# Kernel tuning notes

Hardware: AMD Instinct MI355X
Metric: run time of the kernel (lower is better)

Reference implementation:

```python
import jax, jax.numpy as jnp
import numpy as np

NUM_HEADS = 12
HEAD_DIM = 64
HIDDEN = NUM_HEADS * HEAD_DIM


def setup_inputs() -> dict:
    key = jax.random.key(0)
    ks = jax.random.split(key, 10)
    B, S, N_ROT = 8, 1374, 1369
    s = 0.02
    return {
        "hidden_states": jax.random.normal(ks[0], (B, S, HIDDEN), jnp.float32),
        "sin": jax.random.normal(ks[1], (N_ROT, HEAD_DIM), jnp.float32),
        "cos": jax.random.normal(ks[2], (N_ROT, HEAD_DIM), jnp.float32),
        "Wq": jax.random.normal(ks[3], (HIDDEN, HIDDEN), jnp.float32) * s,
        "bq": jax.random.normal(ks[4], (HIDDEN,), jnp.float32) * s,
        "Wk": jax.random.normal(ks[5], (HIDDEN, HIDDEN), jnp.float32) * s,
        "Wv": jax.random.normal(ks[6], (HIDDEN, HIDDEN), jnp.float32) * s,
        "bv": jax.random.normal(ks[7], (HIDDEN,), jnp.float32) * s,
        "Wp": jax.random.normal(ks[8], (HIDDEN, HIDDEN), jnp.float32) * s,
        "bp": jax.random.normal(ks[9], (HIDDEN,), jnp.float32) * s,
    }


def _rotate_half(x):
    x1, x2 = jnp.split(x, 2, axis=-1)
    return jnp.concatenate([-x2, x1], axis=-1)


def _rope_apply(x, sin, cos):
    return x * cos + _rotate_half(x) * sin


def reference(hidden_states, sin, cos, Wq, bq, Wk, Wv, bv, Wp, bp):
    B, S, _ = hidden_states.shape
    scaling = HEAD_DIM ** -0.5

    def to_heads(x):  # [B,S,HIDDEN] -> [B,H,S,D]
        return x.reshape(B, S, NUM_HEADS, HEAD_DIM).transpose(0, 2, 1, 3)

    q = to_heads(hidden_states @ Wq.T + bq)
    k = to_heads(hidden_states @ Wk.T)  # no key bias (mask_k_bias)
    v = to_heads(hidden_states @ Wv.T + bv)

    # RoPE only on patch tokens (prefix = cls + register tokens untouched)
    prefix = S - sin.shape[-2]
    q = jnp.concatenate([q[:, :, :prefix], _rope_apply(q[:, :, prefix:], sin, cos)], axis=2)
    k = jnp.concatenate([k[:, :, :prefix], _rope_apply(k[:, :, prefix:], sin, cos)], axis=2)

    # eager attention: softmax in float32, no mask, no dropout (eval)
    scores = jnp.einsum("bhqd,bhkd->bhqk", q, k) * scaling
    probs = jax.nn.softmax(scores.astype(jnp.float32), axis=-1).astype(q.dtype)
    ctx = jnp.einsum("bhqk,bhkd->bqhd", probs, v).reshape(B, S, HIDDEN)
    return ctx @ Wp.T + bp
```

## Files before the change

### kernel.cpp

```cpp
#include <hip/hip_runtime.h>
#include <stdint.h>

typedef unsigned short u16;
typedef unsigned int u32;
typedef u16 u16x8 __attribute__((ext_vector_type(8)));
typedef __bf16 bf16x8 __attribute__((ext_vector_type(8)));
typedef float f32x4 __attribute__((ext_vector_type(4)));

#define S_LEN 1374
#define S_PAD 1408
#define PRE_TOK 5
#define HID 768
#define NH 12
#define MPAD 11008

__device__ __forceinline__ u16 f2bf(float f) {
    union { float f; u32 u; } v; v.f = f;
    u32 r = v.u + 0x7fffu + ((v.u >> 16) & 1u);
    return (u16)(r >> 16);
}
__device__ __forceinline__ bf16x8 as_bf(u16x8 v) { bf16x8 r; __builtin_memcpy(&r, &v, 16); return r; }
__device__ __forceinline__ bf16x8 lds_load8(const u16* p) {
    u16x8 t = *(const u16x8*)p;
    return as_bf(t);
}
__device__ __forceinline__ u32 cvtpk_bf16(float lo, float hi) {
    u32 r;
    asm("v_cvt_pk_bf16_f32 %0, %1, %2" : "=v"(r) : "v"(lo), "v"(hi));
    return r;
}
__device__ __forceinline__ float fexp2(float x) {
    float r;
    asm("v_exp_f32 %0, %1" : "=v"(r) : "v"(x));
    return r;
}
__device__ __forceinline__ void gload16(void* lds, const void* g) {
    unsigned int __attribute__((address_space(1)))* gp =
        (unsigned int __attribute__((address_space(1)))*)(unsigned long long)g;
    unsigned int __attribute__((address_space(3)))* lp =
        (unsigned int __attribute__((address_space(3)))*)(unsigned int)(unsigned long long)lds;
    __builtin_amdgcn_global_load_lds(gp, lp, 16, 0, 0);
}
__device__ __forceinline__ int xcd_swz(int orig, int nwg) {
    int qd = nwg >> 3, rd = nwg & 7;
    int xcd = orig & 7, rem = orig >> 3;
    return (xcd < rd ? xcd * (qd + 1) : rd * (qd + 1) + (xcd - rd) * qd) + rem;
}


__global__ __launch_bounds__(256) void pack_x(const float* __restrict__ X, u16* __restrict__ Xb) {
    size_t i = (size_t)blockIdx.x * 256 + threadIdx.x;
    size_t e = i * 8;
    const size_t TOT = (size_t)10992 * HID;
    u16x8 o = {0,0,0,0,0,0,0,0};
    if (e < TOT) {
        f32x4 a = *(const f32x4*)(X + e);
        f32x4 b = *(const f32x4*)(X + e + 4);
#pragma unroll
        for (int j = 0; j < 4; ++j) { o[j] = f2bf(a[j]); o[4 + j] = f2bf(b[j]); }
    }
    *(u16x8*)(Xb + e) = o;
}

__global__ __launch_bounds__(256) void pack_w(
    const float* __restrict__ Wq, const float* __restrict__ Wk, const float* __restrict__ Wv,
    const float* __restrict__ Wp, const float* __restrict__ bq, const float* __restrict__ bv,
    u16* __restrict__ wqkv, u16* __restrict__ wpb, float* __restrict__ bqkv)
{
    int g = blockIdx.x * 256 + threadIdx.x;
    const int QKV8 = 2304 * HID / 8;
    const int P8 = HID * HID / 8;
    if (g < QKV8) {
        int e = g * 8;
        int row = e / HID, col = e - row * HID;
        const float* src = (row < 768) ? (Wq + (size_t)row * HID + col)
                         : (row < 1536) ? (Wk + (size_t)(row - 768) * HID + col)
                                        : (Wv + (size_t)(row - 1536) * HID + col);
        u16x8 o;
#pragma unroll
        for (int j = 0; j < 8; ++j) o[j] = f2bf(src[j]);
        *(u16x8*)(wqkv + e) = o;
    } else if (g < QKV8 + P8) {
        int e = (g - QKV8) * 8;
        u16x8 o;
#pragma unroll
        for (int j = 0; j < 8; ++j) o[j] = f2bf(Wp[e + j]);
        *(u16x8*)(wpb + e) = o;
    }
    if (g < 288) {
        int e = g * 8;
#pragma unroll
        for (int j = 0; j < 8; ++j) {
            int c = e + j;
            bqkv[c] = (c < 768) ? bq[c] : (c < 1536 ? 0.f : bv[c - 1536]);
        }
    }
}


template <int EPI>
__global__ __launch_bounds__(512) void gemm_nt(
    const u16* __restrict__ A, const u16* __restrict__ B, const float* __restrict__ bias,
    float* __restrict__ Yf, u16* __restrict__ Qh, u16* __restrict__ Kh,
    u16* __restrict__ Yv, const float* __restrict__ SN, const float* __restrict__ CS,
    int N, int K, int nx, int nwg)
{
    __shared__ u16 As[128 * 64];
    __shared__ u16 Bs[256 * 64];
    int tid = threadIdx.x;
    int w = tid >> 6, l = tid & 63;
    int fr = l & 15, fg = l >> 4;
    int wg = xcd_swz(blockIdx.x, nwg);
    int col0 = (wg % nx) * 256;
    int row0 = (wg / nx) * 128;
    int wr = (w >> 2) * 64;
    int wc = (w & 3) * 64;

    f32x4 zero4 = {0.f, 0.f, 0.f, 0.f};
    f32x4 acc[4][4];
#pragma unroll
    for (int m = 0; m < 4; ++m)
#pragma unroll
        for (int n = 0; n < 4; ++n) acc[m][n] = zero4;

    int arow[2], aoff[2];
#pragma unroll
    for (int i = 0; i < 2; ++i) {
        int sbyte = (i * 512 + tid) * 16;
        int r = sbyte >> 7;
        int ir = (sbyte & 127) ^ ((r & 7) << 4);
        arow[i] = r; aoff[i] = ir >> 1;
    }
    int brow[4], boff[4];
#pragma unroll
    for (int i = 0; i < 4; ++i) {
        int sbyte = (i * 512 + tid) * 16;
        int r = sbyte >> 7;
        int ir = (sbyte & 127) ^ ((r & 7) << 4);
        brow[i] = r; boff[i] = ir >> 1;
    }

    for (int kt = 0; kt < K; kt += 64) {
#pragma unroll
        for (int i = 0; i < 2; ++i)
            gload16((char*)As + i * 8192 + w * 1024,
                    A + (size_t)(row0 + arow[i]) * K + kt + aoff[i]);
#pragma unroll
        for (int i = 0; i < 4; ++i)
            gload16((char*)Bs + i * 8192 + w * 1024,
                    B + (size_t)(col0 + brow[i]) * K + kt + boff[i]);
        __syncthreads();
#pragma unroll
        for (int c = 0; c < 2; ++c) {
            bf16x8 af[4], bfr[4];
#pragma unroll
            for (int m = 0; m < 4; ++m) {
                int r = wr + m * 16 + fr;
                int byte_ = (c * 64 + fg * 16) ^ ((r & 7) << 4);
                af[m] = lds_load8(As + r * 64 + (byte_ >> 1));
            }
#pragma unroll
            for (int n = 0; n < 4; ++n) {
                int r = wc + n * 16 + fr;
                int byte_ = (c * 64 + fg * 16) ^ ((r & 7) << 4);
                bfr[n] = lds_load8(Bs + r * 64 + (byte_ >> 1));
            }
#pragma unroll
            for (int m = 0; m < 4; ++m)
#pragma unroll
                for (int n = 0; n < 4; ++n)
                    acc[m][n] = __builtin_amdgcn_mfma_f32_16x16x32_bf16(af[m], bfr[n], acc[m][n], 0, 0, 0);
        }
        __syncthreads();
    }

    if (EPI == 1) {
#pragma unroll
        for (int m = 0; m < 4; ++m)
#pragma unroll
            for (int n = 0; n < 4; ++n) {
                int gn = col0 + wc + n * 16 + fr;
                float bvv = bias[gn];
#pragma unroll
                for (int j = 0; j < 4; ++j) {
                    int gm = row0 + wr + m * 16 + fg * 4 + j;
                    if (gm < 10992) Yf[(size_t)gm * N + gn] = acc[m][n][j] + bvv;
                }
            }
    } else {
        int sect = col0 >= 1536 ? 2 : (col0 >= 768 ? 1 : 0);
        if (sect == 2) {
#pragma unroll
            for (int m = 0; m < 4; ++m)
#pragma unroll
                for (int n = 0; n < 4; ++n) {
                    int gn = col0 + wc + n * 16 + fr;
                    float bvv = bias[gn];
#pragma unroll
                    for (int j = 0; j < 4; ++j) {
                        int gm = row0 + wr + m * 16 + fg * 4 + j;
                        if (gm < 10992)
                            Yv[(size_t)gm * HID + (gn - 1536)] = f2bf(acc[m][n][j] + bvv);
                    }
                }
        } else {
            u16* H = sect ? Kh : Qh;
            const float QS = sect ? 1.f : 0.125f * 1.44269504088896f;
            int hh = ((col0 + wc) >> 6) - sect * NH;
            float bv4[4];
#pragma unroll
            for (int n = 0; n < 4; ++n) bv4[n] = bias[col0 + wc + n * 16 + fr];
#pragma unroll
            for (int m = 0; m < 4; ++m)
#pragma unroll
                for (int j = 0; j < 4; ++j) {
                    int gm = row0 + wr + m * 16 + fg * 4 + j;
                    if (gm < 10992) {
                        int b = gm / 1374, s = gm - b * 1374;
                        size_t ob = ((size_t)(b * NH + hh) * S_PAD + s) * 64;
#pragma unroll
                        for (int n2 = 0; n2 < 2; ++n2) {
                            int d = n2 * 16 + fr;
                            float v1 = acc[m][n2][j] + bv4[n2];
                            float v2 = acc[m][n2 + 2][j] + bv4[n2 + 2];
                            float a1 = v1, a2 = v2;
                            if (s >= PRE_TOK) {
                                size_t rr = (size_t)(s - PRE_TOK) * 64;
                                float c1 = CS[rr + d], s1 = SN[rr + d];
                                float c2 = CS[rr + d + 32], s2 = SN[rr + d + 32];
                                a1 = v1 * c1 - v2 * s1;
                                a2 = v2 * c2 + v1 * s2;
                            }
                            H[ob + d]      = f2bf(a1 * QS);
                            H[ob + d + 32] = f2bf(a2 * QS);
                        }
                    }
                }
        }
    }
}


__global__ __launch_bounds__(256) void v_pack(const u16* __restrict__ Yv, u16* __restrict__ Vt) {
    int st = blockIdx.x, bh = blockIdx.y;
    int b = bh / NH, h = bh - b * NH;
    int tid = threadIdx.x;
    int sl = tid >> 2, dg = (tid & 3) * 8;
    int s = st * 64 + sl;
    __shared__ u16 vtile[64 * 64];

    u16x8 a = {0,0,0,0,0,0,0,0}, a2 = {0,0,0,0,0,0,0,0};
    if (s < S_LEN) {
        size_t base = ((size_t)b * S_LEN + s) * HID + h * 64;
        a  = *(const u16x8*)(Yv + base + dg);
        a2 = *(const u16x8*)(Yv + base + 32 + dg);
    }
#pragma unroll
    for (int j = 0; j < 8; ++j) {
        vtile[(dg + j) * 64 + sl] = a[j];
        vtile[(32 + dg + j) * 64 + sl] = a2[j];
    }
    __syncthreads();
    int d = tid >> 2, so = (tid & 3) * 8;
    u16x8 ov0 = *(const u16x8*)(vtile + d * 64 + so);
    u16x8 ov1 = *(const u16x8*)(vtile + d * 64 + so + 32);
    size_t vrow = ((size_t)bh * 64 + d) * S_PAD + st * 64;
    *(u16x8*)(Vt + vrow + so) = ov0;
    *(u16x8*)(Vt + vrow + so + 32) = ov1;
}


#define FLASH_BODY(Kc, Vc, KsN, VsN, ktn, DO_STAGE, DO_MASK)                          \
    {                                                                                 \
        asm volatile("s_waitcnt vmcnt(0) lgkmcnt(0)" ::: "memory");                   \
        __syncthreads();                                                              \
        if (DO_STAGE) {                                                               \
            int k0n = (ktn) * 32;                                                     \
            gload16((char*)(KsN) + sb, Kb + (size_t)k0n * 64 + kfix);                 \
            gload16((char*)(VsN) + sb, Vb + (size_t)k0n + vfix);                      \
        }                                                                             \
        f32x4 sf[2][2];                                                               \
        __builtin_amdgcn_s_setprio(1);                                                \
        _Pragma("unroll")                                                             \
        for (int n = 0; n < 2; ++n) {                                                 \
            f32x4 q0a = zero4, q1a = zero4;                                           \
            _Pragma("unroll")                                                         \
            for (int c = 0; c < 2; ++c) {                                             \
                int byte_ = (c * 64 + fg * 16) ^ ((fr & 7) << 4);                     \
                bf16x8 kf = lds_load8((Kc) + (n * 16 + fr) * 64 + (byte_ >> 1));      \
                q0a = __builtin_amdgcn_mfma_f32_16x16x32_bf16(kf, qf[0][c], q0a, 0, 0, 0); \
                q1a = __builtin_amdgcn_mfma_f32_16x16x32_bf16(kf, qf[1][c], q1a, 0, 0, 0); \
            }                                                                         \
            sf[0][n] = q0a; sf[1][n] = q1a;                                           \
        }                                                                             \
        __builtin_amdgcn_s_setprio(0);                                                \
        if (DO_MASK) {                                                                \
            _Pragma("unroll")                                                         \
            for (int n = 0; n < 2; ++n)                                               \
                _Pragma("unroll")                                                     \
                for (int j = 0; j < 4; ++j)                                           \
                    if (1344 + 8 * fg + 4 * n + j >= S_LEN) {                         \
                        sf[0][n][j] = -1e30f; sf[1][n][j] = -1e30f;                   \
                    }                                                                 \
        }                                                                             \
        union PA { u32 w2[4]; bf16x8 v; } pa[2];                                      \
        _Pragma("unroll")                                                             \
        for (int qq = 0; qq < 2; ++qq) {                                              \
            _Pragma("unroll")                                                         \
            for (int n = 0; n < 2; ++n)                                               \
                _Pragma("unroll")                                                     \
                for (int j = 0; j < 4; ++j) sf[qq][n][j] = fexp2(sf[qq][n][j]);       \
            pa[qq].w2[0] = cvtpk_bf16(sf[qq][0][0], sf[qq][0][1]);                    \
            pa[qq].w2[1] = cvtpk_bf16(sf[qq][0][2], sf[qq][0][3]);                    \
            pa[qq].w2[2] = cvtpk_bf16(sf[qq][1][0], sf[qq][1][1]);                    \
            pa[qq].w2[3] = cvtpk_bf16(sf[qq][1][2], sf[qq][1][3]);                    \
        }                                                                             \
        __builtin_amdgcn_s_setprio(1);                                                \
        lsum0 = __builtin_amdgcn_mfma_f32_16x16x32_bf16(pa[0].v, ones, lsum0, 0, 0, 0); \
        lsum1 = __builtin_amdgcn_mfma_f32_16x16x32_bf16(pa[1].v, ones, lsum1, 0, 0, 0); \
        _Pragma("unroll")                                                             \
        for (int nd = 0; nd < 4; ++nd) {                                              \
            int byte_ = ((nd >> 1) * 64 + fg * 16) ^ ((fr & 7) << 4);                 \
            bf16x8 vf = lds_load8((Vc) + ((nd & 1) * 16 + fr) * 64 + (byte_ >> 1));   \
            octx[0][nd] = __builtin_amdgcn_mfma_f32_16x16x32_bf16(pa[0].v, vf, octx[0][nd], 0, 0, 0); \
            octx[1][nd] = __builtin_amdgcn_mfma_f32_16x16x32_bf16(pa[1].v, vf, octx[1][nd], 0, 0, 0); \
        }                                                                             \
        __builtin_amdgcn_s_setprio(0);                                                \
    }

__global__ __launch_bounds__(256, 4) void flash(
    const u16* __restrict__ Qh, const u16* __restrict__ Kh, const u16* __restrict__ Vt,
    u16* __restrict__ ctxO)
{
    int wg = (blockIdx.x & 7) * 132 + (blockIdx.x >> 3);
    int qt = wg % 11, bh = wg / 11;
    int b = bh / NH, h = bh - b * NH;
    int q0 = qt * 128;
    int tid = threadIdx.x, w = tid >> 6, l = tid & 63;
    int fr = l & 15, fg = l >> 4;

    __shared__ u16 Ks0[32 * 64], Ks1[32 * 64];
    __shared__ u16 Vs0[32 * 64], Vs1[32 * 64];

    const u16* Qb = Qh + (size_t)bh * S_PAD * 64;
    const u16* Kb = Kh + (size_t)bh * S_PAD * 64;
    const u16* Vb = Vt + (size_t)bh * 64 * S_PAD;

    bf16x8 qf[2][2];
#pragma unroll
    for (int qq = 0; qq < 2; ++qq) {
        int qrow = q0 + w * 32 + qq * 16 + fr;
#pragma unroll
        for (int c = 0; c < 2; ++c)
            qf[qq][c] = as_bf(*(const u16x8*)(Qb + (size_t)qrow * 64 + c * 32 + fg * 8));
    }

    u16x8 ones_u = {0x3F80, 0x3F80, 0x3F80, 0x3F80, 0x3F80, 0x3F80, 0x3F80, 0x3F80};
    bf16x8 ones = as_bf(ones_u);

    f32x4 zero4 = {0.f, 0.f, 0.f, 0.f};
    f32x4 octx[2][4];
#pragma unroll
    for (int qq = 0; qq < 2; ++qq)
#pragma unroll
        for (int nd = 0; nd < 4; ++nd) octx[qq][nd] = zero4;
    f32x4 lsum0 = zero4, lsum1 = zero4;

    int r = w * 8 + (l >> 3);
    int bb = (l & 7) * 16;
    int ir = bb ^ ((r & 7) << 4);
    int gk = ((r >> 2) & 3) * 8 + ((r >> 4) & 1) * 4 + (r & 3);
    int kfix = gk * 64 + (ir >> 1);
    int vfix = (r + (ir >> 6) * 32) * S_PAD + ((ir & 63) >> 1);
    int sb = w * 1024;

    gload16((char*)Ks0 + sb, Kb + kfix);
    gload16((char*)Vs0 + sb, Vb + vfix);

    for (int kt = 0; kt < 42; kt += 2) {
        FLASH_BODY(Ks0, Vs0, Ks1, Vs1, kt + 1, true, false);
        FLASH_BODY(Ks1, Vs1, Ks0, Vs0, kt + 2, true, false);
    }
    FLASH_BODY(Ks0, Vs0, Ks1, Vs1, 0, false, true);

#pragma unroll
    for (int qq = 0; qq < 2; ++qq)
#pragma unroll
        for (int j = 0; j < 4; ++j) {
            int q = q0 + w * 32 + qq * 16 + fg * 4 + j;
            if (q < S_LEN) {
                float lv = qq ? lsum1[j] : lsum0[j];
                float inv = 1.f / lv;
                size_t rowb = ((size_t)b * S_LEN + q) * HID + h * 64;
#pragma unroll
                for (int nd = 0; nd < 4; ++nd)
                    ctxO[rowb + nd * 16 + fr] = f2bf(octx[qq][nd][j] * inv);
            }
        }
}


extern "C" void kernel_launch(void* const* d_in, const int* in_sizes, int n_in,
                              void* d_out, int out_size, void* d_ws, size_t ws_size,
                              hipStream_t stream) {
    (void)in_sizes; (void)n_in; (void)out_size; (void)ws_size;
    const float* X  = (const float*)d_in[0];
    const float* SN = (const float*)d_in[1];
    const float* CS = (const float*)d_in[2];
    const float* Wq = (const float*)d_in[3];
    const float* bq = (const float*)d_in[4];
    const float* Wk = (const float*)d_in[5];
    const float* Wv = (const float*)d_in[6];
    const float* bv = (const float*)d_in[7];
    const float* Wp = (const float*)d_in[8];
    const float* bp = (const float*)d_in[9];
    float* OUT = (float*)d_out;
    char* ws = (char*)d_ws;

    u16*   xb   = (u16*)(ws);
    u16*   wqkv = (u16*)(ws + 16908288);
    u16*   wpb  = (u16*)(ws + 20447232);
    float* bqkv = (float*)(ws + 21626880);
    u16*   Yv   = (u16*)(ws + 21636096);
    u16*   Qh   = (u16*)(ws + 72360960);
    u16*   Kh   = (u16*)(ws + 89662464);
    u16*   Vt   = (u16*)(ws + 106963968);
    u16*   ctx  = xb;

    pack_x<<<4128, 256, 0, stream>>>(X, xb);
    pack_w<<<1152, 256, 0, stream>>>(Wq, Wk, Wv, Wp, bq, bv, wqkv, wpb, bqkv);
    gemm_nt<2><<<774, 512, 0, stream>>>(xb, wqkv, bqkv, nullptr, Qh, Kh, Yv, SN, CS, 2304, 768, 9, 774);
    v_pack<<<dim3(22, 96), 256, 0, stream>>>(Yv, Vt);
    flash<<<1056, 256, 0, stream>>>(Qh, Kh, Vt, ctx);
    gemm_nt<1><<<258, 512, 0, stream>>>(ctx, wpb, bp, OUT, nullptr, nullptr, nullptr, nullptr, nullptr, 768, 768, 3, 258);
}
```

Measured before the change: 167.3 us.

## Use 64-key tiles in flash attention and merge pack kernels

The flash kernel now stages 64 keys per double-buffered step instead of 32. Each step does two 32-key sub-blocks, so there are half as many barriers and waitcnt stalls per KV pass, and shared memory grows to 32KB per block. The x and weight packing kernels are merged into one launch to save launch overhead. The larger LDS footprint could reduce occupancy, and the last iteration now masks keys against the 1344+64 tail.

```diff
diff --git a/kernel.cpp b/kernel.cpp
--- a/kernel.cpp
+++ b/kernel.cpp
@@ -48,26 +48,29 @@
 }
 
 
-__global__ __launch_bounds__(256) void pack_x(const float* __restrict__ X, u16* __restrict__ Xb) {
-    size_t i = (size_t)blockIdx.x * 256 + threadIdx.x;
-    size_t e = i * 8;
-    const size_t TOT = (size_t)10992 * HID;
-    u16x8 o = {0,0,0,0,0,0,0,0};
-    if (e < TOT) {
-        f32x4 a = *(const f32x4*)(X + e);
-        f32x4 b = *(const f32x4*)(X + e + 4);
-#pragma unroll
-        for (int j = 0; j < 4; ++j) { o[j] = f2bf(a[j]); o[4 + j] = f2bf(b[j]); }
-    }
-    *(u16x8*)(Xb + e) = o;
-}
-
-__global__ __launch_bounds__(256) void pack_w(
-    const float* __restrict__ Wq, const float* __restrict__ Wk, const float* __restrict__ Wv,
-    const float* __restrict__ Wp, const float* __restrict__ bq, const float* __restrict__ bv,
+__global__ __launch_bounds__(256) void pack_xw(
+    const float* __restrict__ X, const float* __restrict__ Wq, const float* __restrict__ Wk,
+    const float* __restrict__ Wv, const float* __restrict__ Wp, const float* __restrict__ bq,
+    const float* __restrict__ bv, u16* __restrict__ Xb,
     u16* __restrict__ wqkv, u16* __restrict__ wpb, float* __restrict__ bqkv)
 {
-    int g = blockIdx.x * 256 + threadIdx.x;
+    int bid = blockIdx.x;
+    int tid = threadIdx.x;
+    if (bid < 4128) {
+        size_t i = (size_t)bid * 256 + tid;
+        size_t e = i * 8;
+        const size_t TOT = (size_t)10992 * HID;
+        u16x8 o = {0,0,0,0,0,0,0,0};
+        if (e < TOT) {
+            f32x4 a = *(const f32x4*)(X + e);
+            f32x4 b = *(const f32x4*)(X + e + 4);
+#pragma unroll
+            for (int j = 0; j < 4; ++j) { o[j] = f2bf(a[j]); o[4 + j] = f2bf(b[j]); }
+        }
+        *(u16x8*)(Xb + e) = o;
+        return;
+    }
+    int g = (bid - 4128) * 256 + tid;
     const int QKV8 = 2304 * HID / 8;
     const int P8 = HID * HID / 8;
     if (g < QKV8) {
@@ -270,62 +273,68 @@
 }
 
 
-#define FLASH_BODY(Kc, Vc, KsN, VsN, ktn, DO_STAGE, DO_MASK)                          \
+#define FLASH_B64(Kc, Vc, KsN, VsN, ktn, DO_STAGE, DO_MASK)                           \
     {                                                                                 \
         asm volatile("s_waitcnt vmcnt(0) lgkmcnt(0)" ::: "memory");                   \
         __syncthreads();                                                              \
         if (DO_STAGE) {                                                               \
-            int k0n = (ktn) * 32;                                                     \
-            gload16((char*)(KsN) + sb, Kb + (size_t)k0n * 64 + kfix);                 \
-            gload16((char*)(VsN) + sb, Vb + (size_t)k0n + vfix);                      \
+            int k0n = (ktn) * 64;                                                     \
+            _Pragma("unroll")                                                         \
+            for (int i = 0; i < 2; ++i) {                                             \
+                gload16((char*)(KsN) + i * 4096 + w * 1024, Kb + (size_t)k0n * 64 + kfix[i]); \
+                gload16((char*)(VsN) + i * 4096 + w * 1024, Vb + (size_t)k0n + vfix[i]);      \
+            }                                                                         \
         }                                                                             \
-        f32x4 sf[2][2];                                                               \
-        __builtin_amdgcn_s_setprio(1);                                                \
         _Pragma("unroll")                                                             \
-        for (int n = 0; n < 2; ++n) {                                                 \
-            f32x4 q0a = zero4, q1a = zero4;                                           \
+        for (int h = 0; h < 2; ++h) {                                                 \
+            f32x4 sf[2][2];                                                           \
+            __builtin_amdgcn_s_setprio(1);                                            \
             _Pragma("unroll")                                                         \
-            for (int c = 0; c < 2; ++c) {                                             \
-                int byte_ = (c * 64 + fg * 16) ^ ((fr & 7) << 4);                     \
-                bf16x8 kf = lds_load8((Kc) + (n * 16 + fr) * 64 + (byte_ >> 1));      \
-                q0a = __builtin_amdgcn_mfma_f32_16x16x32_bf16(kf, qf[0][c], q0a, 0, 0, 0); \
-                q1a = __builtin_amdgcn_mfma_f32_16x16x32_bf16(kf, qf[1][c], q1a, 0, 0, 0); \
+            for (int n = 0; n < 2; ++n) {                                             \
+                f32x4 q0a = zero4, q1a = zero4;                                       \
+                _Pragma("unroll")                                                     \
+                for (int c = 0; c < 2; ++c) {                                         \
+                    int byte_ = (c * 64 + fg * 16) ^ ((fr & 7) << 4);                 \
+                    bf16x8 kf = lds_load8((Kc) + (h * 32 + n * 16 + fr) * 64 + (byte_ >> 1)); \
+                    q0a = __builtin_amdgcn_mfma_f32_16x16x32_bf16(kf, qf[0][c], q0a, 0, 0, 0); \
+                    q1a = __builtin_amdgcn_mfma_f32_16x16x32_bf16(kf, qf[1][c], q1a, 0, 0, 0); \
+                }                                                                     \
+                sf[0][n] = q0a; sf[1][n] = q1a;                                       \
             }                                                                         \
-            sf[0][n] = q0a; sf[1][n] = q1a;                                           \
+            __builtin_amdgcn_s_setprio(0);                                            \
+            if (DO_MASK) {                                                            \
+                _Pragma("unroll")                                                     \
+                for (int n = 0; n < 2; ++n)                                           \
+                    _Pragma("unroll")                                                 \
+                    for (int j = 0; j < 4; ++j)                                       \
+                        if (1344 + h * 32 + 8 * fg + 4 * n + j >= S_LEN) {            \
+                            sf[0][n][j] = -1e30f; sf[1][n][j] = -1e30f;               \
+                        }                                                             \
+            }                                                                         \
+            union PA { u32 w2[4]; bf16x8 v; } pa[2];                                  \
+            _Pragma("unroll")                                                         \
+            for (int qq = 0; qq < 2; ++qq) {                                          \
+                _Pragma("unroll")                                                     \
+                for (int n = 0; n < 2; ++n)                                           \
+                    _Pragma("unroll")                                                 \
+                    for (int j = 0; j < 4; ++j) sf[qq][n][j] = fexp2(sf[qq][n][j]);   \
+                pa[qq].w2[0] = cvtpk_bf16(sf[qq][0][0], sf[qq][0][1]);                \
+                pa[qq].w2[1] = cvtpk_bf16(sf[qq][0][2], sf[qq][0][3]);                \
+                pa[qq].w2[2] = cvtpk_bf16(sf[qq][1][0], sf[qq][1][1]);                \
+                pa[qq].w2[3] = cvtpk_bf16(sf[qq][1][2], sf[qq][1][3]);                \
+            }                                                                         \
+            __builtin_amdgcn_s_setprio(1);                                            \
+            lsum0 = __builtin_amdgcn_mfma_f32_16x16x32_bf16(pa[0].v, ones, lsum0, 0, 0, 0); \
+            lsum1 = __builtin_amdgcn_mfma_f32_16x16x32_bf16(pa[1].v, ones, lsum1, 0, 0, 0); \
+            _Pragma("unroll")                                                         \
+            for (int nd = 0; nd < 4; ++nd) {                                          \
+                int byte_ = (h * 64 + fg * 16) ^ ((fr & 7) << 4);                     \
+                bf16x8 vf = lds_load8((Vc) + (nd * 16 + fr) * 64 + (byte_ >> 1));     \
+                octx[0][nd] = __builtin_amdgcn_mfma_f32_16x16x32_bf16(pa[0].v, vf, octx[0][nd], 0, 0, 0); \
+                octx[1][nd] = __builtin_amdgcn_mfma_f32_16x16x32_bf16(pa[1].v, vf, octx[1][nd], 0, 0, 0); \
+            }                                                                         \
+            __builtin_amdgcn_s_setprio(0);                                            \
         }                                                                             \
-        __builtin_amdgcn_s_setprio(0);                                                \
-        if (DO_MASK) {                                                                \
-            _Pragma("unroll")                                                         \
-            for (int n = 0; n < 2; ++n)                                               \
-                _Pragma("unroll")                                                     \
-                for (int j = 0; j < 4; ++j)                                           \
-                    if (1344 + 8 * fg + 4 * n + j >= S_LEN) {                         \
-                        sf[0][n][j] = -1e30f; sf[1][n][j] = -1e30f;                   \
-                    }                                                                 \
-        }                                                                             \
-        union PA { u32 w2[4]; bf16x8 v; } pa[2];                                      \
-        _Pragma("unroll")                                                             \
-        for (int qq = 0; qq < 2; ++qq) {                                              \
-            _Pragma("unroll")                                                         \
-            for (int n = 0; n < 2; ++n)                                               \
-                _Pragma("unroll")                                                     \
-                for (int j = 0; j < 4; ++j) sf[qq][n][j] = fexp2(sf[qq][n][j]);       \
-            pa[qq].w2[0] = cvtpk_bf16(sf[qq][0][0], sf[qq][0][1]);                    \
-            pa[qq].w2[1] = cvtpk_bf16(sf[qq][0][2], sf[qq][0][3]);                    \
-            pa[qq].w2[2] = cvtpk_bf16(sf[qq][1][0], sf[qq][1][1]);                    \
-            pa[qq].w2[3] = cvtpk_bf16(sf[qq][1][2], sf[qq][1][3]);                    \
-        }                                                                             \
-        __builtin_amdgcn_s_setprio(1);                                                \
-        lsum0 = __builtin_amdgcn_mfma_f32_16x16x32_bf16(pa[0].v, ones, lsum0, 0, 0, 0); \
-        lsum1 = __builtin_amdgcn_mfma_f32_16x16x32_bf16(pa[1].v, ones, lsum1, 0, 0, 0); \
-        _Pragma("unroll")                                                             \
-        for (int nd = 0; nd < 4; ++nd) {                                              \
-            int byte_ = ((nd >> 1) * 64 + fg * 16) ^ ((fr & 7) << 4);                 \
-            bf16x8 vf = lds_load8((Vc) + ((nd & 1) * 16 + fr) * 64 + (byte_ >> 1));   \
-            octx[0][nd] = __builtin_amdgcn_mfma_f32_16x16x32_bf16(pa[0].v, vf, octx[0][nd], 0, 0, 0); \
-            octx[1][nd] = __builtin_amdgcn_mfma_f32_16x16x32_bf16(pa[1].v, vf, octx[1][nd], 0, 0, 0); \
-        }                                                                             \
-        __builtin_amdgcn_s_setprio(0);                                                \
     }
 
 __global__ __launch_bounds__(256, 4) void flash(
@@ -339,8 +348,8 @@
     int tid = threadIdx.x, w = tid >> 6, l = tid & 63;
     int fr = l & 15, fg = l >> 4;
 
-    __shared__ u16 Ks0[32 * 64], Ks1[32 * 64];
-    __shared__ u16 Vs0[32 * 64], Vs1[32 * 64];
+    __shared__ u16 Ks0[64 * 64], Ks1[64 * 64];
+    __shared__ u16 Vs0[64 * 64], Vs1[64 * 64];
 
     const u16* Qb = Qh + (size_t)bh * S_PAD * 64;
     const u16* Kb = Kh + (size_t)bh * S_PAD * 64;
@@ -366,22 +375,32 @@
         for (int nd = 0; nd < 4; ++nd) octx[qq][nd] = zero4;
     f32x4 lsum0 = zero4, lsum1 = zero4;
 
-    int r = w * 8 + (l >> 3);
-    int bb = (l & 7) * 16;
-    int ir = bb ^ ((r & 7) << 4);
-    int gk = ((r >> 2) & 3) * 8 + ((r >> 4) & 1) * 4 + (r & 3);
-    int kfix = gk * 64 + (ir >> 1);
-    int vfix = (r + (ir >> 6) * 32) * S_PAD + ((ir & 63) >> 1);
-    int sb = w * 1024;
-
-    gload16((char*)Ks0 + sb, Kb + kfix);
-    gload16((char*)Vs0 + sb, Vb + vfix);
-
-    for (int kt = 0; kt < 42; kt += 2) {
-        FLASH_BODY(Ks0, Vs0, Ks1, Vs1, kt + 1, true, false);
-        FLASH_BODY(Ks1, Vs1, Ks0, Vs0, kt + 2, true, false);
-    }
-    FLASH_BODY(Ks0, Vs0, Ks1, Vs1, 0, false, true);
+    int kfix[2], vfix[2];
+#pragma unroll
+    for (int i = 0; i < 2; ++i) {
+        int sby = (i * 256 + tid) * 16;
+        int r = sby >> 7;
+        int ir = (sby & 127) ^ ((r & 7) << 4);
+        int r5 = r & 31;
+        int gk = (r >> 5) * 32 + 8 * ((r5 >> 2) & 3) + 4 * (r5 >> 4) + (r5 & 3);
+        kfix[i] = gk * 64 + (ir >> 1);
+        vfix[i] = r * S_PAD + (ir >> 1);
+    }
+
+    {
+#pragma unroll
+        for (int i = 0; i < 2; ++i) {
+            gload16((char*)Ks0 + i * 4096 + w * 1024, Kb + kfix[i]);
+            gload16((char*)Vs0 + i * 4096 + w * 1024, Vb + vfix[i]);
+        }
+    }
+
+    for (int kt = 0; kt < 20; kt += 2) {
+        FLASH_B64(Ks0, Vs0, Ks1, Vs1, kt + 1, true, false);
+        FLASH_B64(Ks1, Vs1, Ks0, Vs0, kt + 2, true, false);
+    }
+    FLASH_B64(Ks0, Vs0, Ks1, Vs1, 21, true, false);
+    FLASH_B64(Ks1, Vs1, Ks0, Vs0, 0, false, true);
 
 #pragma unroll
     for (int qq = 0; qq < 2; ++qq)
@@ -427,8 +446,7 @@
     u16*   Vt   = (u16*)(ws + 106963968);
     u16*   ctx  = xb;
 
-    pack_x<<<4128, 256, 0, stream>>>(X, xb);
-    pack_w<<<1152, 256, 0, stream>>>(Wq, Wk, Wv, Wp, bq, bv, wqkv, wpb, bqkv);
+    pack_xw<<<5280, 256, 0, stream>>>(X, Wq, Wk, Wv, Wp, bq, bv, xb, wqkv, wpb, bqkv);
     gemm_nt<2><<<774, 512, 0, stream>>>(xb, wqkv, bqkv, nullptr, Qh, Kh, Yv, SN, CS, 2304, 768, 9, 774);
     v_pack<<<dim3(22, 96), 256, 0, stream>>>(Yv, Vt);
     flash<<<1056, 256, 0, stream>>>(Qh, Kh, Vt, ctx);
```

Measured after the change: 166.3 us, median of 4. No clear change (-0.6%).
